# Optimization experiments

Measured on AMD Instinct MI355X. Metric: run time of the kernel, lower is better.

## Reference

```python
import jax, jax.numpy as jnp
import numpy as np
import math

B, K, T = 4, 1024, 2048
OD, H = 128, 8


def setup_inputs() -> dict:
    key = jax.random.key(0)
    ks = jax.random.split(key, 6)
    s_in = 1.0 / math.sqrt(K)
    s_u = 1.0 / math.sqrt(H * OD)
    return {
        "x": jax.random.normal(ks[0], (B, K, T), dtype=jnp.float32),
        "Wk": jax.random.uniform(ks[1], (H * OD, K), minval=-s_in, maxval=s_in, dtype=jnp.float32),
        "Wq": jax.random.uniform(ks[2], (H * OD, K), minval=-s_in, maxval=s_in, dtype=jnp.float32),
        "Wv": jax.random.uniform(ks[3], (H * OD, K), minval=-s_in, maxval=s_in, dtype=jnp.float32),
        "Wu": jax.random.uniform(ks[4], (OD, H * OD), minval=-s_u, maxval=s_u, dtype=jnp.float32),
        "bu": jax.random.uniform(ks[5], (OD,), minval=-s_u, maxval=s_u, dtype=jnp.float32),
    }


def reference(x, Wk, Wq, Wv, Wu, bu):
    b, k, t = x.shape
    # QKV projections: Linear applied over channel dim of channels-first input
    keys = jnp.einsum('bkt,jk->bjt', x, Wk).reshape(b, H, OD, t)
    queries = jnp.einsum('bkt,jk->bjt', x, Wq).reshape(b, H, OD, t)
    values = jnp.einsum('bkt,jk->bjt', x, Wv).reshape(b, H, OD, t)
    # attention scores over time: [b, h, t, t]
    dot = jnp.einsum('bhkt,bhki->bhti', queries, keys) / math.sqrt(OD)
    dot = jax.nn.softmax(dot, axis=-1)
    out = jnp.einsum('bhti,bhki->bhkt', dot, values)  # [b, h, od, t]
    # unify heads: weight (OD, H*OD) viewed as (OD_out=k, H=h, OD=e)
    out = jnp.einsum('bhet,khe->bkt', out, Wu.reshape(OD, H, OD))
    return out + bu[None, :, None]
```

## Files before the change

### kernel.cpp

```cpp
#include <hip/hip_runtime.h>
#include <hip/hip_bf16.h>
#include <type_traits>
#include <utility>

#define DEVINL __device__ __forceinline__

typedef unsigned short u16;
typedef unsigned int   u32;
typedef short  s8v  __attribute__((ext_vector_type(8)));
typedef __bf16 b8v  __attribute__((ext_vector_type(8)));
typedef float  f4v  __attribute__((ext_vector_type(4)));
typedef float  f16v __attribute__((ext_vector_type(16)));
typedef u32    u4v  __attribute__((ext_vector_type(4)));

static constexpr int BB = 4, KD = 1024, TT = 2048, OD = 128, NH = 8;
static constexpr int J2 = 2048;

template<class V, class = void> struct mfma_takes : std::false_type {};
template<class V> struct mfma_takes<V, std::void_t<decltype(
    __builtin_amdgcn_mfma_f32_16x16x32_bf16(std::declval<V>(), std::declval<V>(),
                                            std::declval<f4v>(), 0, 0, 0))>> : std::true_type {};

template<class AV>
DEVINL f4v mfma16(AV a, AV b, f4v c) {
  if constexpr (mfma_takes<AV>::value) {
    return __builtin_amdgcn_mfma_f32_16x16x32_bf16(a, b, c, 0, 0, 0);
  } else {
    return __builtin_amdgcn_mfma_f32_16x16x32_bf16(
        __builtin_bit_cast(b8v, a), __builtin_bit_cast(b8v, b), c, 0, 0, 0);
  }
}

template<class V, class = void> struct mfma32_takes : std::false_type {};
template<class V> struct mfma32_takes<V, std::void_t<decltype(
    __builtin_amdgcn_mfma_f32_32x32x16_bf16(std::declval<V>(), std::declval<V>(),
                                            std::declval<f16v>(), 0, 0, 0))>> : std::true_type {};

template<class AV>
DEVINL f16v mfma32(AV a, AV b, f16v c) {
  if constexpr (mfma32_takes<AV>::value) {
    return __builtin_amdgcn_mfma_f32_32x32x16_bf16(a, b, c, 0, 0, 0);
  } else {
    return __builtin_amdgcn_mfma_f32_32x32x16_bf16(
        __builtin_bit_cast(b8v, a), __builtin_bit_cast(b8v, b), c, 0, 0, 0);
  }
}

DEVINL u16 f2bf(float f) {
  union { float f; u32 u; } v; v.f = f;
  u32 u = v.u;
  return (u16)((u + 0x7fffu + ((u >> 16) & 1u)) >> 16);
}
DEVINL float bf2f(u16 h) { union { u32 u; float f; } v; v.u = ((u32)h) << 16; return v.f; }

DEVINL u32 cvtpk_bf16(float a, float b) {
  u32 r;
  asm("v_cvt_pk_bf16_f32 %0, %1, %2" : "=v"(r) : "v"(a), "v"(b));
  return r;
}

DEVINL void gload_lds16(const void* g, void* l) {
  __builtin_amdgcn_global_load_lds(
      (const __attribute__((address_space(1))) void*)g,
      (__attribute__((address_space(3))) void*)l, 16, 0, 0);
}

__global__ void xpose_split_x(const float* __restrict__ x, u16* __restrict__ xTh) {
  __shared__ float tile[32][33];
  const int b  = blockIdx.z;
  const int k0 = blockIdx.y * 32;
  const int t0 = blockIdx.x * 32;
  const int tx = threadIdx.x;
  const int ty = threadIdx.y;
  const float* xb = x + (size_t)b * KD * TT;
#pragma unroll
  for (int j = 0; j < 4; ++j)
    tile[ty + j * 8][tx] = xb[(size_t)(k0 + ty + j * 8) * TT + t0 + tx];
  __syncthreads();
  u16* oh = xTh + (size_t)b * TT * KD;
#pragma unroll
  for (int j = 0; j < 4; ++j) {
    int t = ty + j * 8;
    float v = tile[tx][t];
    oh[(size_t)(t0 + t) * KD + k0 + tx] = f2bf(v);
  }
}

__global__ void split_weights(const float* __restrict__ Wk, const float* __restrict__ Wq,
                              const float* __restrict__ Wv, const float* __restrict__ Wu,
                              u16* __restrict__ Wkqh, u16* __restrict__ Wvh,
                              u16* __restrict__ Wuh,  u16* __restrict__ Wul,
                              float qscale) {
  int i = blockIdx.x * 256 + threadIdx.x;
  if (i < 1048576) {
    Wkqh[i] = f2bf(Wk[i]);
    Wkqh[1048576 + i] = f2bf(Wq[i] * qscale);
    Wvh[i] = f2bf(Wv[i]);
    if (i < 131072) {
      float v = Wu[i];  u16 hh = f2bf(v);
      Wuh[i] = hh;      Wul[i] = f2bf(v - bf2f(hh));
    }
  }
}

template<int EPI>
__global__ __launch_bounds__(256, 3) void gemm_bt_split(
    const u16* __restrict__ Ahi, const u16* __restrict__ Alo,
    const u16* __restrict__ Bhi, const u16* __restrict__ Blo,
    void* __restrict__ Couth,
    const float* __restrict__ bias,
    int Kdim, int ldc, long strideA, long strideB, long strideC, int npass) {
  __shared__ __align__(16) u16 At[128 * 64];
  __shared__ __align__(16) u16 Bt[128 * 64];
  const int tid = threadIdx.x;
  const int w = tid >> 6, l = tid & 63;
  const int wm = w >> 1, wn = w & 1;
  const int lr = l & 15, lg = l >> 4;
  const int b = blockIdx.z;
  const u16* Ah = Ahi + (size_t)b * strideA;
  const u16* Al = Alo ? Alo + (size_t)b * strideA : nullptr;
  const u16* Bh = Bhi + (size_t)b * strideB;
  const u16* Bl = Blo ? Blo + (size_t)b * strideB : nullptr;
  const int m0 = blockIdx.x * 128;
  const int n0 = (EPI == 3) ? ((blockIdx.y & 15) * 128) : (blockIdx.y * 128);
  const int ky = (EPI == 3) ? (blockIdx.y >> 4) : 0;
  const int kspan = (EPI == 3) ? (Kdim / 2) : Kdim;
  const int kbase = ky * kspan;

  int srow[4], soff[4];
#pragma unroll
  for (int i = 0; i < 4; ++i) {
    int c = tid + i * 256;
    int row = c >> 3, q = c & 7;
    srow[i] = row;
    soff[i] = (q ^ (row & 7)) * 8;
  }

  f4v acc[4][4] = {};

  const int spi = kspan / 64;
  const int iters = npass * spi;
  for (int it = 0; it < iters; ++it) {
    const int seg = it / spi;
    const int k = kbase + (it - seg * spi) * 64;
    const u16* As = (seg == 2) ? Al : Ah;
    const u16* Bs = (seg == 1) ? Bl : Bh;
#pragma unroll
    for (int i = 0; i < 4; ++i) {
      int c = tid + i * 256;
      gload_lds16(As + (size_t)(m0 + srow[i]) * Kdim + k + soff[i], (char*)At + c * 16);
      gload_lds16(Bs + (size_t)(n0 + srow[i]) * Kdim + k + soff[i], (char*)Bt + c * 16);
    }
    __syncthreads();
    __builtin_amdgcn_s_setprio(1);
#pragma unroll
    for (int kk = 0; kk < 2; ++kk) {
      const int q = kk * 4 + lg;
      s8v a[4], bb[4];
#pragma unroll
      for (int mi = 0; mi < 4; ++mi) {
        int row = wm * 64 + mi * 16 + lr;
        a[mi] = *(const s8v*)(&At[row * 64 + (q ^ (row & 7)) * 8]);
      }
#pragma unroll
      for (int ni = 0; ni < 4; ++ni) {
        int row = wn * 64 + ni * 16 + lr;
        bb[ni] = *(const s8v*)(&Bt[row * 64 + (q ^ (row & 7)) * 8]);
      }
#pragma unroll
      for (int mi = 0; mi < 4; ++mi)
#pragma unroll
        for (int ni = 0; ni < 4; ++ni)
          acc[mi][ni] = mfma16(a[mi], bb[ni], acc[mi][ni]);
    }
    __builtin_amdgcn_s_setprio(0);
    __syncthreads();
  }

  if constexpr (EPI == 2) {
    u16* Ch = (u16*)Couth + (size_t)b * strideC;
#pragma unroll
    for (int mi = 0; mi < 4; ++mi)
#pragma unroll
      for (int ni = 0; ni < 4; ++ni)
#pragma unroll
        for (int r = 0; r < 4; ++r) {
          int m = m0 + wm * 64 + mi * 16 + lg * 4 + r;
          int n = n0 + wn * 64 + ni * 16 + lr;
          Ch[(size_t)m * ldc + n] = f2bf(acc[mi][ni][r]);
        }
  } else if constexpr (EPI == 3) {
    float* C = (float*)Couth + ((size_t)ky * BB + b) * strideC;
#pragma unroll
    for (int mi = 0; mi < 4; ++mi)
#pragma unroll
      for (int ni = 0; ni < 4; ++ni)
#pragma unroll
        for (int r = 0; r < 4; ++r) {
          int m = m0 + wm * 64 + mi * 16 + lg * 4 + r;
          int n = n0 + wn * 64 + ni * 16 + lr;
          C[(size_t)m * ldc + n] = acc[mi][ni][r];
        }
  } else {
    float* C = (float*)Couth + (size_t)b * strideC;
#pragma unroll
    for (int mi = 0; mi < 4; ++mi)
#pragma unroll
      for (int ni = 0; ni < 4; ++ni)
#pragma unroll
        for (int r = 0; r < 4; ++r) {
          int m = m0 + wm * 64 + mi * 16 + lg * 4 + r;
          int n = n0 + wn * 64 + ni * 16 + lr;
          C[(size_t)m * ldc + n] = acc[mi][ni][r] + bias[m];
        }
  }
}

__global__ void addbias(const float* __restrict__ part, float* __restrict__ out,
                        const float* __restrict__ bias) {
  int i = blockIdx.x * 256 + threadIdx.x;
  f4v a = ((const f4v*)part)[i];
  f4v c = ((const f4v*)part)[i + 262144];
  float bs = bias[(i >> 9) & 127];
  f4v r;
#pragma unroll
  for (int j = 0; j < 4; ++j) r[j] = a[j] + c[j] + bs;
  ((f4v*)out)[i] = r;
}

__global__ __launch_bounds__(256, 2) void attn_fwd(
    const u16* __restrict__ QKTh, const u16* __restrict__ Vh,
    u16* __restrict__ OTh, u16* __restrict__ OTl) {
  __shared__ __align__(16) u16 Ksh[2][32 * 128];
  __shared__ __align__(16) u16 Vsh[2][128 * 32];

  const int bid = blockIdx.x;
  const int lid = (bid & 7) * 64 + (bid >> 3);
  const int t0 = (lid & 15) * 128;
  const int h  = (lid >> 4) & 7;
  const int b  = lid >> 7;

  const int tid = threadIdx.x;
  const int w = tid >> 6, l = tid & 63;
  const int lw = l & 31, hi = l >> 5;
  const size_t qb = (size_t)b * TT * J2;
  const u16* Qh_ = QKTh + qb + 1024 + h * 128;
  const u16* Kh_ = QKTh + qb + h * 128;
  const u16* Vh_ = Vh + (size_t)b * 1024 * TT + (size_t)h * 128 * TT;

  int koff[2], kdo[2], voff[2], vdo[2];
#pragma unroll
  for (int i = 0; i < 2; ++i) {
    int c = tid + i * 256;
    { int row = c >> 4, q = c & 15;
      koff[i] = row * J2 + (q ^ (row & 7)) * 8;  kdo[i] = c * 16; }
    { int row = c >> 2, q = c & 3;
      voff[i] = row * TT + (q ^ ((row >> 1) & 3)) * 8;  vdo[i] = c * 16; }
  }

#define ATTN_STAGE(BSEL, I0) do {                                          \
    _Pragma("unroll")                                                      \
    for (int i_ = 0; i_ < 2; ++i_) {                                       \
      gload_lds16(Kh_ + (size_t)(I0) * J2 + koff[i_], (char*)Ksh[BSEL] + kdo[i_]); \
      gload_lds16(Vh_ + voff[i_] + (I0),              (char*)Vsh[BSEL] + vdo[i_]); \
    } } while (0)

  s8v qh[8];
  {
    const size_t trow = (size_t)(t0 + w * 32 + lw) * J2;
#pragma unroll
    for (int st = 0; st < 8; ++st)
      qh[st] = *(const s8v*)(Qh_ + trow + st * 16 + hi * 8);
  }

  f16v o[4] = {};
  float lsum = 0.f;

  ATTN_STAGE(0, 0);

  for (int it = 0; it < 64; ++it) {
    const int cur = it & 1;
    if (it + 1 < 64) {
      ATTN_STAGE(cur ^ 1, (it + 1) * 32);
      asm volatile("s_waitcnt vmcnt(4)" ::: "memory");
    } else {
      asm volatile("s_waitcnt vmcnt(0)" ::: "memory");
    }
    __builtin_amdgcn_s_barrier();

    const u16* Ks = Ksh[cur];
    const u16* Vs = Vsh[cur];
    f16v s0 = {}, s1 = {};
    __builtin_amdgcn_s_setprio(1);
#pragma unroll
    for (int st = 0; st < 4; ++st) {
      s8v kf0 = *(const s8v*)(&Ks[lw * 128 + (((st * 2 + hi) ^ (lw & 7)) * 8)]);
      s8v kf1 = *(const s8v*)(&Ks[lw * 128 + ((((st + 4) * 2 + hi) ^ (lw & 7)) * 8)]);
      s0 = mfma32(kf0, qh[st], s0);
      s1 = mfma32(kf1, qh[st + 4], s1);
    }
    __builtin_amdgcn_s_setprio(0);

    u32 wp[4][2];
    float ps = 0.f;
#pragma unroll
    for (int g = 0; g < 4; ++g) {
      float e0 = exp2f(s0[g * 4 + 0] + s1[g * 4 + 0]);
      float e1 = exp2f(s0[g * 4 + 1] + s1[g * 4 + 1]);
      float e2 = exp2f(s0[g * 4 + 2] + s1[g * 4 + 2]);
      float e3 = exp2f(s0[g * 4 + 3] + s1[g * 4 + 3]);
      ps += (e0 + e1) + (e2 + e3);
      wp[g][0] = cvtpk_bf16(e0, e1);
      wp[g][1] = cvtpk_bf16(e2, e3);
    }
    lsum += ps;

    s8v pa[2];
#pragma unroll
    for (int ks = 0; ks < 2; ++ks) {
      u32 a0 = wp[2 * ks][0], b0 = wp[2 * ks + 1][0];
      u32 a1 = wp[2 * ks][1], b1 = wp[2 * ks + 1][1];
      asm volatile("v_permlane32_swap_b32 %0, %1" : "+v"(a0), "+v"(b0));
      asm volatile("v_permlane32_swap_b32 %0, %1" : "+v"(a1), "+v"(b1));
      u4v fw; fw[0] = a0; fw[1] = a1; fw[2] = b0; fw[3] = b1;
      pa[ks] = __builtin_bit_cast(s8v, fw);
    }

    __builtin_amdgcn_s_setprio(1);
#pragma unroll
    for (int ks = 0; ks < 2; ++ks) {
#pragma unroll
      for (int et = 0; et < 4; ++et) {
        const int vrow = et * 32 + lw;
        s8v vh = *(const s8v*)(&Vs[vrow * 32 +
                                   (((ks * 2 + hi) ^ ((vrow >> 1) & 3)) * 8)]);
        o[et] = mfma32(pa[ks], vh, o[et]);
      }
    }
    __builtin_amdgcn_s_setprio(0);
    if (it + 1 < 64)
      __builtin_amdgcn_s_barrier();
  }
#undef ATTN_STAGE

  lsum += __shfl_xor(lsum, 32);

  u16* oh = OTh + (size_t)b * TT * 1024;
  u16* ol = OTl + (size_t)b * TT * 1024;
#pragma unroll
  for (int r = 0; r < 16; ++r) {
    const int qrow = (r & 3) + 8 * (r >> 2) + 4 * hi;
    float ls = __shfl(lsum, qrow);
    float inv = 1.0f / ls;
    int t = t0 + w * 32 + qrow;
#pragma unroll
    for (int et = 0; et < 4; ++et) {
      int he = h * 128 + et * 32 + lw;
      float v = o[et][r] * inv;
      u16 hh = f2bf(v);
      oh[(size_t)t * 1024 + he] = hh;
      ol[(size_t)t * 1024 + he] = f2bf(v - bf2f(hh));
    }
  }
}

extern "C" void kernel_launch(void* const* d_in, const int* in_sizes, int n_in,
                              void* d_out, int out_size, void* d_ws, size_t ws_size,
                              hipStream_t stream) {
  const float* x  = (const float*)d_in[0];
  const float* Wk = (const float*)d_in[1];
  const float* Wq = (const float*)d_in[2];
  const float* Wv = (const float*)d_in[3];
  const float* Wu = (const float*)d_in[4];
  const float* bu = (const float*)d_in[5];
  float* out = (float*)d_out;

  const size_t need_bytes = 2ull * (8388608ull + 2097152ull + 1048576ull +
                                    131072ull * 2 + 16777216ull + 8388608ull +
                                    8388608ull * 2 + 4194304ull);
  if (ws_size < need_bytes) {
    (void)hipMemsetAsync(d_out, 0, (size_t)out_size * sizeof(float), stream);
    return;
  }
  u16* p = (u16*)d_ws;
  u16* xTh = p;  p += 8388608;
  u16* Wkqh = p; p += 2097152;
  u16* Wvh = p;  p += 1048576;
  u16* Wuh = p;  p += 131072;
  u16* Wul = p;  p += 131072;
  u16* QKTh = p; p += 16777216;
  u16* Vh = p;   p += 8388608;
  u16* OTh = p;  p += 8388608;
  u16* OTl = p;  p += 8388608;
  float* Cpart = (float*)p; p += 4194304;

  const float qscale = 0.08838834764831845f * 1.4426950408889634f;

  xpose_split_x<<<dim3(64, 32, 4), dim3(32, 8), 0, stream>>>(x, xTh);
  split_weights<<<4096, 256, 0, stream>>>(Wk, Wq, Wv, Wu, Wkqh, Wvh, Wuh, Wul, qscale);

  gemm_bt_split<2><<<dim3(16, 16, 4), 256, 0, stream>>>(
      xTh, nullptr, Wkqh, nullptr, QKTh, nullptr,
      1024, 2048, 2097152L, 0L, 4194304L, 1);
  gemm_bt_split<2><<<dim3(8, 16, 4), 256, 0, stream>>>(
      Wvh, nullptr, xTh, nullptr, Vh, nullptr,
      1024, 2048, 0L, 2097152L, 2097152L, 1);
  attn_fwd<<<dim3(512), dim3(256), 0, stream>>>(QKTh, Vh, OTh, OTl);
  gemm_bt_split<3><<<dim3(1, 32, 4), 256, 0, stream>>>(
      Wuh, Wul, OTh, OTl, Cpart, nullptr,
      1024, 2048, 0L, 2097152L, 262144L, 3);
  addbias<<<1024, 256, 0, stream>>>(Cpart, out, bu);
}
```

Measured before the change: 198.1 us.

## Split attention over key halves and combine partials; drop low-bf16 O split

The attention kernel now splits the key/time dimension into two halves, doubling the grid to 1024 blocks. Each block writes unnormalized fp32 partial outputs and row sums, and a new combine kernel sums the halves, normalizes, and writes bf16 O. The softmax has no running max, so the two halves share a scale and can simply be added. The output projection GEMM drops the low-bf16 correction term for O, going from 3 passes to 2. This trades more parallelism and less unify-GEMM work for a large fp32 partial buffer round-trip and an extra launch, and loses some precision in O.

```diff
diff --git a/kernel.cpp b/kernel.cpp
--- a/kernel.cpp
+++ b/kernel.cpp
@@ -143,8 +143,8 @@
   for (int it = 0; it < iters; ++it) {
     const int seg = it / spi;
     const int k = kbase + (it - seg * spi) * 64;
-    const u16* As = (seg == 2) ? Al : Ah;
-    const u16* Bs = (seg == 1) ? Bl : Bh;
+    const u16* As = (seg == 2 || (seg == 1 && npass == 2)) ? Al : Ah;
+    const u16* Bs = (seg == 1 && npass == 3) ? Bl : Bh;
 #pragma unroll
     for (int i = 0; i < 4; ++i) {
       int c = tid + i * 256;
@@ -230,15 +230,17 @@
 
 __global__ __launch_bounds__(256, 2) void attn_fwd(
     const u16* __restrict__ QKTh, const u16* __restrict__ Vh,
-    u16* __restrict__ OTh, u16* __restrict__ OTl) {
+    float* __restrict__ opart, float* __restrict__ lpart) {
   __shared__ __align__(16) u16 Ksh[2][32 * 128];
   __shared__ __align__(16) u16 Vsh[2][128 * 32];
 
   const int bid = blockIdx.x;
-  const int lid = (bid & 7) * 64 + (bid >> 3);
+  const int lid = (bid & 7) * 128 + (bid >> 3);
   const int t0 = (lid & 15) * 128;
-  const int h  = (lid >> 4) & 7;
-  const int b  = lid >> 7;
+  const int kh = (lid >> 4) & 1;
+  const int h  = (lid >> 5) & 7;
+  const int b  = lid >> 8;
+  const int base = kh << 10;
 
   const int tid = threadIdx.x;
   const int w = tid >> 6, l = tid & 63;
@@ -276,12 +278,12 @@
   f16v o[4] = {};
   float lsum = 0.f;
 
-  ATTN_STAGE(0, 0);
-
-  for (int it = 0; it < 64; ++it) {
+  ATTN_STAGE(0, base);
+
+  for (int it = 0; it < 32; ++it) {
     const int cur = it & 1;
-    if (it + 1 < 64) {
-      ATTN_STAGE(cur ^ 1, (it + 1) * 32);
+    if (it + 1 < 32) {
+      ATTN_STAGE(cur ^ 1, base + (it + 1) * 32);
       asm volatile("s_waitcnt vmcnt(4)" ::: "memory");
     } else {
       asm volatile("s_waitcnt vmcnt(0)" ::: "memory");
@@ -338,30 +340,48 @@
       }
     }
     __builtin_amdgcn_s_setprio(0);
-    if (it + 1 < 64)
+    if (it + 1 < 32)
       __builtin_amdgcn_s_barrier();
   }
 #undef ATTN_STAGE
 
   lsum += __shfl_xor(lsum, 32);
-
-  u16* oh = OTh + (size_t)b * TT * 1024;
-  u16* ol = OTl + (size_t)b * TT * 1024;
+  if (l < 32)
+    lpart[(((size_t)kh * 4 + b) * 8 + h) * 2048 + t0 + w * 32 + l] = lsum;
+
+  float* op = opart + ((size_t)kh * 4 + b) * (2048 * 1024);
 #pragma unroll
   for (int r = 0; r < 16; ++r) {
     const int qrow = (r & 3) + 8 * (r >> 2) + 4 * hi;
-    float ls = __shfl(lsum, qrow);
-    float inv = 1.0f / ls;
     int t = t0 + w * 32 + qrow;
 #pragma unroll
     for (int et = 0; et < 4; ++et) {
       int he = h * 128 + et * 32 + lw;
-      float v = o[et][r] * inv;
-      u16 hh = f2bf(v);
-      oh[(size_t)t * 1024 + he] = hh;
-      ol[(size_t)t * 1024 + he] = f2bf(v - bf2f(hh));
-    }
-  }
+      op[(size_t)t * 1024 + he] = o[et][r];
+    }
+  }
+}
+
+__global__ void combine_o(const float* __restrict__ opart, const float* __restrict__ lpart,
+                          u16* __restrict__ OTh) {
+  int i = blockIdx.x * 256 + threadIdx.x;
+  int he4 = i & 255;
+  int t   = (i >> 8) & 2047;
+  int b   = i >> 19;
+  int h   = he4 >> 5;
+  size_t o0 = (size_t)i;
+  size_t o1 = o0 + (size_t)4 * 2048 * 256;
+  f4v a = ((const f4v*)opart)[o0];
+  f4v c = ((const f4v*)opart)[o1];
+  float lsum = lpart[((size_t)b * 8 + h) * 2048 + t] +
+               lpart[(((size_t)4 + b) * 8 + h) * 2048 + t];
+  float inv = 1.0f / lsum;
+  ushort4 r;
+  r.x = f2bf((a[0] + c[0]) * inv);
+  r.y = f2bf((a[1] + c[1]) * inv);
+  r.z = f2bf((a[2] + c[2]) * inv);
+  r.w = f2bf((a[3] + c[3]) * inv);
+  *(ushort4*)(OTh + (size_t)i * 4) = r;
 }
 
 extern "C" void kernel_launch(void* const* d_in, const int* in_sizes, int n_in,
@@ -377,7 +397,7 @@
 
   const size_t need_bytes = 2ull * (8388608ull + 2097152ull + 1048576ull +
                                     131072ull * 2 + 16777216ull + 8388608ull +
-                                    8388608ull * 2 + 4194304ull);
+                                    8388608ull + 33554432ull + 262144ull + 4194304ull);
   if (ws_size < need_bytes) {
     (void)hipMemsetAsync(d_out, 0, (size_t)out_size * sizeof(float), stream);
     return;
@@ -391,8 +411,9 @@
   u16* QKTh = p; p += 16777216;
   u16* Vh = p;   p += 8388608;
   u16* OTh = p;  p += 8388608;
-  u16* OTl = p;  p += 8388608;
-  float* Cpart = (float*)p; p += 4194304;
+  float* opart = (float*)p; p += 33554432;
+  float* lpart = (float*)p; p += 262144;
+  float* Cpart = (float*)p; p += 8388608;
 
   const float qscale = 0.08838834764831845f * 1.4426950408889634f;
 
@@ -405,9 +426,10 @@
   gemm_bt_split<2><<<dim3(8, 16, 4), 256, 0, stream>>>(
       Wvh, nullptr, xTh, nullptr, Vh, nullptr,
       1024, 2048, 0L, 2097152L, 2097152L, 1);
-  attn_fwd<<<dim3(512), dim3(256), 0, stream>>>(QKTh, Vh, OTh, OTl);
+  attn_fwd<<<dim3(1024), dim3(256), 0, stream>>>(QKTh, Vh, opart, lpart);
+  combine_o<<<dim3(8192), dim3(256), 0, stream>>>(opart, lpart, OTh);
   gemm_bt_split<3><<<dim3(1, 32, 4), 256, 0, stream>>>(
-      Wuh, Wul, OTh, OTl, Cpart, nullptr,
-      1024, 2048, 0L, 2097152L, 262144L, 3);
+      Wuh, Wul, OTh, nullptr, Cpart, nullptr,
+      1024, 2048, 0L, 2097152L, 262144L, 2);
   addbias<<<1024, 256, 0, stream>>>(Cpart, out, bu);
 }
```

Result: slower. 207.9 us (+5.0%).
